# Performance work log

Hardware: AMD Instinct MI355X
Metric: run time of the kernel (lower is better)

Reference implementation:

```python
import jax, jax.numpy as jnp
import numpy as np

# Dimensions: T total tokens, D encoder dim, M mentions, E entities, L_MAX max span length
T, D, M, E, L_MAX = 200000, 256, 20000, 4000, 16


def setup_inputs() -> dict:
    key = jax.random.key(0)
    k1, k2, k3 = jax.random.split(key, 3)
    enc_seq = jax.random.normal(k1, (T, D), dtype=jnp.float32)
    starts = jax.random.randint(k2, (M,), 0, T - L_MAX)
    lens = jax.random.randint(k3, (M,), 1, L_MAX + 1)
    ends = starts + lens
    # entity ids: every entity gets at least one mention (matches max(info[:,0])+1 entities)
    eids = jnp.arange(M, dtype=jnp.int32) % E
    etype = jnp.zeros((M,), dtype=jnp.int32)
    info = jnp.stack([eids, etype, starts, ends], axis=1).astype(jnp.int64)
    return {"enc_seq": enc_seq, "info": info, "num_entities": E}


def reference(enc_seq, info, num_entities):
    # --- merge_tokens: mean-pool contiguous token spans into mentions ---
    starts = info[:, 2]
    ends = info[:, 3]
    lens = (ends - starts)  # [M]
    offs = jnp.arange(L_MAX)  # spans are at most L_MAX tokens
    idx = starts[:, None] + offs[None, :]            # [M, L_MAX]
    mask = offs[None, :] < lens[:, None]             # [M, L_MAX]
    tok = enc_seq[idx]                               # [M, L_MAX, D] gather
    mentions = jnp.sum(jnp.where(mask[:, :, None], tok, 0.0), axis=1)
    mentions = mentions / lens[:, None].astype(enc_seq.dtype)  # exact span mean

    # --- merge_mentions: mean-pool mentions sharing an entity id into entities ---
    eid = info[:, 0]
    ent_sum = jax.ops.segment_sum(mentions, eid, num_segments=num_entities)       # [E, D]
    cnt = jax.ops.segment_sum(jnp.ones((M,), enc_seq.dtype), eid,
                              num_segments=num_entities)                          # [E]
    entities = ent_sum / jnp.maximum(cnt, 1.0)[:, None]
    return entities
```

## Files before the change

kernel.cpp:

```cpp
#include <hip/hip_runtime.h>

#define DDIM 256
#define WAVES_PER_BLOCK 4


__global__ void scatter_kernel(const int* __restrict__ info,
                               int* __restrict__ cursor,
                               int* __restrict__ bucket,
                               int M) {
    int m = blockIdx.x * blockDim.x + threadIdx.x;
    if (m >= M) return;
    int eid = info[(size_t)m * 4];
    int pos = atomicAdd(cursor + eid, 1);
    bucket[(size_t)eid * M + pos] = m;
}

__global__ void entity_kernel(const float* __restrict__ enc,
                              const int* __restrict__ info,
                              const int* __restrict__ cursor,
                              const int* __restrict__ bucket,
                              float* __restrict__ out,
                              int M, int E) {
    int e = blockIdx.x * WAVES_PER_BLOCK + (threadIdx.x >> 6);
    if (e >= E) return;
    int lane = threadIdx.x & 63;

    int cnt = cursor[e];
    const int* bk = bucket + (size_t)e * M;

    float4 eacc = make_float4(0.f, 0.f, 0.f, 0.f);
    for (int j = 0; j < cnt; ++j) {
        int m = bk[j];
        const int* r = info + (size_t)m * 4;
        int start = r[2];
        int len   = r[3] - start;
        const float4* base = reinterpret_cast<const float4*>(enc)
                             + (size_t)start * (DDIM / 4) + lane;
        float4 macc = make_float4(0.f, 0.f, 0.f, 0.f);
        for (int i = 0; i < len; ++i) {
            float4 v = base[(size_t)i * (DDIM / 4)];
            macc.x += v.x; macc.y += v.y; macc.z += v.z; macc.w += v.w;
        }
        float inv = (len > 0) ? 1.0f / (float)len : 0.0f;
        eacc.x += macc.x * inv; eacc.y += macc.y * inv;
        eacc.z += macc.z * inv; eacc.w += macc.w * inv;
    }
    float invc = 1.0f / fmaxf((float)cnt, 1.0f);
    float4 res = make_float4(eacc.x * invc, eacc.y * invc,
                             eacc.z * invc, eacc.w * invc);
    reinterpret_cast<float4*>(out + (size_t)e * DDIM)[lane] = res;
}


__global__ void mention_accum_kernel(const float* __restrict__ enc,
                                     const int* __restrict__ info,
                                     float* __restrict__ ent_sum,
                                     float* __restrict__ cnt,
                                     int M) {
    int wave = blockIdx.x * WAVES_PER_BLOCK + (threadIdx.x >> 6);
    if (wave >= M) return;
    int lane = threadIdx.x & 63;
    const int* r = info + (size_t)wave * 4;
    int eid = r[0], start = r[2], len = r[3] - r[2];
    if (len <= 0) {
        if (lane == 0) atomicAdd(cnt + eid, 1.0f);
        return;
    }
    const float4* base = reinterpret_cast<const float4*>(enc)
                         + (size_t)start * (DDIM / 4) + lane;
    float4 acc = make_float4(0.f, 0.f, 0.f, 0.f);
    for (int i = 0; i < len; ++i) {
        float4 v = base[(size_t)i * (DDIM / 4)];
        acc.x += v.x; acc.y += v.y; acc.z += v.z; acc.w += v.w;
    }
    float inv = 1.0f / (float)len;
    float* dst = ent_sum + (size_t)eid * DDIM + lane * 4;
    atomicAdd(dst + 0, acc.x * inv);
    atomicAdd(dst + 1, acc.y * inv);
    atomicAdd(dst + 2, acc.z * inv);
    atomicAdd(dst + 3, acc.w * inv);
    if (lane == 0) atomicAdd(cnt + eid, 1.0f);
}

__global__ void finalize_kernel(float* __restrict__ out,
                                const float* __restrict__ cnt, int n) {
    int t = blockIdx.x * blockDim.x + threadIdx.x;
    if (t >= n) return;
    out[t] = out[t] / fmaxf(cnt[t >> 8], 1.0f);
}

extern "C" void kernel_launch(void* const* d_in, const int* in_sizes, int n_in,
                              void* d_out, int out_size, void* d_ws, size_t ws_size,
                              hipStream_t stream) {
    const float* enc  = (const float*)d_in[0];
    const int*   info = (const int*)d_in[1];

    int M = in_sizes[1] / 4;
    int E = out_size / DDIM;
    float* out = (float*)d_out;

    size_t cursor_bytes = 16384;
    size_t need = cursor_bytes + (size_t)E * (size_t)M * sizeof(int);

    if (ws_size >= need) {
        int* cursor = (int*)d_ws;
        int* bucket = (int*)((char*)d_ws + cursor_bytes);

        hipMemsetAsync(cursor, 0, (size_t)E * sizeof(int), stream);
        scatter_kernel<<<(M + 255) / 256, 256, 0, stream>>>(info, cursor, bucket, M);
        int blocks = (E + WAVES_PER_BLOCK - 1) / WAVES_PER_BLOCK;
        entity_kernel<<<blocks, 64 * WAVES_PER_BLOCK, 0, stream>>>(
            enc, info, cursor, bucket, out, M, E);
    } else {
        float* cnt = (float*)d_ws;
        hipMemsetAsync(d_out, 0, (size_t)out_size * sizeof(float), stream);
        hipMemsetAsync(cnt, 0, (size_t)E * sizeof(float), stream);
        int blocks = (M + WAVES_PER_BLOCK - 1) / WAVES_PER_BLOCK;
        mention_accum_kernel<<<blocks, 64 * WAVES_PER_BLOCK, 0, stream>>>(
            enc, info, out, cnt, M);
        finalize_kernel<<<(out_size + 255) / 256, 256, 0, stream>>>(out, cnt, out_size);
    }
}
```

Measured before the change: 43.52 us.

## Split each entity across two waves and batch mention metadata loads via shuffles

The entity kernel now assigns two waves per entity, each handling half of the feature dimension with float2 loads, which doubles the wave count available to hide gather latency. Mention indices and span bounds are loaded cooperatively, one per lane, in chunks of 64 and broadcast with shuffles, so the serial per-mention bucket and info loads go away. The inner token loop is unrolled by four. In exchange, each wave re-reads the bucket and info entries, and the narrower float2 loads issue more memory instructions per byte.

```diff
diff --git a/kernel.cpp b/kernel.cpp
--- a/kernel.cpp
+++ b/kernel.cpp
@@ -2,6 +2,7 @@
 
 #define DDIM 256
 #define WAVES_PER_BLOCK 4
+#define HALVES 2
 
 
 __global__ void scatter_kernel(const int* __restrict__ info,
@@ -21,34 +22,47 @@
                               const int* __restrict__ bucket,
                               float* __restrict__ out,
                               int M, int E) {
-    int e = blockIdx.x * WAVES_PER_BLOCK + (threadIdx.x >> 6);
+    int gw = blockIdx.x * WAVES_PER_BLOCK + (threadIdx.x >> 6);
+    int e    = gw / HALVES;
+    int half = gw % HALVES;
     if (e >= E) return;
     int lane = threadIdx.x & 63;
 
     int cnt = cursor[e];
     const int* bk = bucket + (size_t)e * M;
 
-    float4 eacc = make_float4(0.f, 0.f, 0.f, 0.f);
-    for (int j = 0; j < cnt; ++j) {
-        int m = bk[j];
-        const int* r = info + (size_t)m * 4;
-        int start = r[2];
-        int len   = r[3] - start;
-        const float4* base = reinterpret_cast<const float4*>(enc)
-                             + (size_t)start * (DDIM / 4) + lane;
-        float4 macc = make_float4(0.f, 0.f, 0.f, 0.f);
-        for (int i = 0; i < len; ++i) {
-            float4 v = base[(size_t)i * (DDIM / 4)];
-            macc.x += v.x; macc.y += v.y; macc.z += v.z; macc.w += v.w;
+    const int COLS2 = DDIM / 2;
+    const int HW    = DDIM / (2 * HALVES);
+
+    float2 eacc = make_float2(0.f, 0.f);
+    for (int j0 = 0; j0 < cnt; j0 += 64) {
+        int nj = min(cnt - j0, 64);
+        int mystart = 0, mylen = 0;
+        if (lane < nj) {
+            int m = bk[j0 + lane];
+            int4 r = reinterpret_cast<const int4*>(info)[m];
+            mystart = r.z;
+            mylen   = r.w - r.z;
         }
-        float inv = (len > 0) ? 1.0f / (float)len : 0.0f;
-        eacc.x += macc.x * inv; eacc.y += macc.y * inv;
-        eacc.z += macc.z * inv; eacc.w += macc.w * inv;
+        for (int j = 0; j < nj; ++j) {
+            int start = __shfl(mystart, j);
+            int len   = __shfl(mylen, j);
+            const float2* base = reinterpret_cast<const float2*>(enc)
+                                 + (size_t)start * COLS2 + half * HW + lane;
+            float2 macc = make_float2(0.f, 0.f);
+            #pragma unroll 4
+            for (int i = 0; i < len; ++i) {
+                float2 v = base[(size_t)i * COLS2];
+                macc.x += v.x; macc.y += v.y;
+            }
+            float inv = (len > 0) ? 1.0f / (float)len : 0.0f;
+            eacc.x += macc.x * inv;
+            eacc.y += macc.y * inv;
+        }
     }
     float invc = 1.0f / fmaxf((float)cnt, 1.0f);
-    float4 res = make_float4(eacc.x * invc, eacc.y * invc,
-                             eacc.z * invc, eacc.w * invc);
-    reinterpret_cast<float4*>(out + (size_t)e * DDIM)[lane] = res;
+    float2 res = make_float2(eacc.x * invc, eacc.y * invc);
+    reinterpret_cast<float2*>(out)[(size_t)e * COLS2 + half * HW + lane] = res;
 }
 
 
@@ -108,7 +122,8 @@
 
         hipMemsetAsync(cursor, 0, (size_t)E * sizeof(int), stream);
         scatter_kernel<<<(M + 255) / 256, 256, 0, stream>>>(info, cursor, bucket, M);
-        int blocks = (E + WAVES_PER_BLOCK - 1) / WAVES_PER_BLOCK;
+        int gwaves = E * HALVES;
+        int blocks = (gwaves + WAVES_PER_BLOCK - 1) / WAVES_PER_BLOCK;
         entity_kernel<<<blocks, 64 * WAVES_PER_BLOCK, 0, stream>>>(
             enc, info, cursor, bucket, out, M, E);
     } else {
```

Measured after the change: 40.78 us. -6.3%, faster.
